# Kernel tuning notes

Measured on AMD Instinct MI355X. Metric: run time of the kernel, lower is better.

The kernel has to match this reference:

```python
import jax, jax.numpy as jnp
from jax import lax
import numpy as np

STRIDE = 16
PRE_NMS = 2000
POST_NMS = 300
NMS_THRESH = 0.7
MIN_SIZE = 16.0  # * img_scale (=1.0)
DN = ('NCHW', 'OIHW', 'NCHW')


def _anchor_base(base=16, ratios=(0.5, 1.0, 2.0), scales=(8, 16, 32)):
    py = px = base / 2.0
    ab = np.zeros((len(ratios) * len(scales), 4), np.float32)
    k = 0
    for r in ratios:
        for s in scales:
            h = base * s * np.sqrt(r)
            w = base * s * np.sqrt(1.0 / r)
            ab[k] = [py - h / 2, px - w / 2, py + h / 2, px + w / 2]
            k += 1
    return ab


def _all_anchors(H, W, img_h, img_w):
    base = _anchor_base()
    sy = np.arange(H, dtype=np.float32) * STRIDE
    sx = np.arange(W, dtype=np.float32) * STRIDE
    yy, xx = np.meshgrid(sy, sx, indexing='ij')
    shifts = np.stack([yy, xx, yy, xx], axis=-1).reshape(-1, 1, 4)
    anchors = (shifts + base[None]).reshape(-1, 4).astype(np.float32)  # (H*W*9, 4)
    valid = np.where((anchors[:, 0] >= 0) & (anchors[:, 1] >= 0) &
                     (anchors[:, 2] <= img_h) & (anchors[:, 3] <= img_w))[0]
    return anchors, valid


def _loc2bbox(anc, loc):
    # anc: (1,K,4), loc: (B,K,4); boxes as (y1,x1,y2,x2)
    h = anc[..., 2] - anc[..., 0]
    w = anc[..., 3] - anc[..., 1]
    cy = anc[..., 0] + 0.5 * h
    cx = anc[..., 1] + 0.5 * w
    ncy = loc[..., 0] * h + cy
    ncx = loc[..., 1] * w + cx
    nh = h * jnp.exp(loc[..., 2])
    nw = w * jnp.exp(loc[..., 3])
    return jnp.stack([ncy - 0.5 * nh, ncx - 0.5 * nw,
                      ncy + 0.5 * nh, ncx + 0.5 * nw], axis=-1)


def _nms(boxes, scores):
    # boxes: (N,4), scores: (N,) -> (POST_NMS,4) zero-padded rois
    areas = (boxes[:, 2] - boxes[:, 0]) * (boxes[:, 3] - boxes[:, 1])

    def step(s, _):
        i = jnp.argmax(s)
        ok = s[i] > -jnp.inf
        b = boxes[i]
        yy1 = jnp.maximum(b[0], boxes[:, 0])
        xx1 = jnp.maximum(b[1], boxes[:, 1])
        yy2 = jnp.minimum(b[2], boxes[:, 2])
        xx2 = jnp.minimum(b[3], boxes[:, 3])
        inter = jnp.maximum(yy2 - yy1, 0.0) * jnp.maximum(xx2 - xx1, 0.0)
        iou = inter / (areas[i] + areas - inter + 1e-9)
        s = jnp.where(iou > NMS_THRESH, -jnp.inf, s).at[i].set(-jnp.inf)
        return s, (i, ok)

    _, (idx, ok) = lax.scan(step, scores, None, length=POST_NMS)
    return boxes[idx] * ok[:, None].astype(boxes.dtype)


def _conv(x, w, b, padding):
    y = lax.conv_general_dilated(x, w, (1, 1), padding, dimension_numbers=DN)
    return y + b[None, :, None, None]


def setup_inputs():
    key = jax.random.key(0)
    k = jax.random.split(key, 4)
    B, C, H, W = 2, 512, 64, 64
    std = 0.01
    return {
        'feat': jax.random.normal(k[0], (B, C, H, W), jnp.float32),
        'share_w': jax.random.normal(k[1], (512, 512, 3, 3), jnp.float32) * std,
        'share_b': jnp.zeros((512,), jnp.float32),
        'cls_w': jax.random.normal(k[2], (18, 512, 1, 1), jnp.float32) * std,
        'cls_b': jnp.zeros((18,), jnp.float32),
        'reg_w': jax.random.normal(k[3], (36, 512, 1, 1), jnp.float32) * std,
        'reg_b': jnp.zeros((36,), jnp.float32),
        'img_h': 1024,
        'img_w': 1024,
    }


def reference(feat, share_w, share_b, cls_w, cls_b, reg_w, reg_b, img_h, img_w):
    B, _, H, W = feat.shape
    anchors_np, valid_np = _all_anchors(H, W, img_h, img_w)
    anchors = jnp.asarray(anchors_np)
    valid = jnp.asarray(valid_np)

    shared = jax.nn.relu(_conv(feat, share_w, share_b, 'SAME'))
    cls = _conv(shared, cls_w, cls_b, 'VALID')   # (B,18,H,W)
    reg = _conv(shared, reg_w, reg_b, 'VALID')   # (B,36,H,W)

    # permute(0,2,3,1).view(-1,2), gather valid anchors, softmax
    cls = cls.transpose(0, 2, 3, 1).reshape(B, -1, 2)[:, valid]   # (B,K,2)
    cls = jax.nn.softmax(cls, axis=-1)
    reg = reg.transpose(0, 2, 3, 1).reshape(B, -1, 4)[:, valid]   # (B,K,4)

    # proposal layer: decode, clip, min-size filter, top-k, NMS
    anc = anchors[valid][None]                                    # (1,K,4)
    boxes = _loc2bbox(anc, reg)                                   # (B,K,4)
    boxes = jnp.stack([jnp.clip(boxes[..., 0], 0.0, img_h),
                       jnp.clip(boxes[..., 1], 0.0, img_w),
                       jnp.clip(boxes[..., 2], 0.0, img_h),
                       jnp.clip(boxes[..., 3], 0.0, img_w)], axis=-1)
    hs = boxes[..., 2] - boxes[..., 0]
    ws = boxes[..., 3] - boxes[..., 1]
    scores = jnp.where((hs >= MIN_SIZE) & (ws >= MIN_SIZE), cls[..., 1], -jnp.inf)

    top_s, top_i = lax.top_k(scores, PRE_NMS)                     # (B,PRE_NMS)
    top_boxes = jnp.take_along_axis(boxes, top_i[..., None], axis=1)
    rois = jax.vmap(_nms)(top_boxes, top_s)                       # (B,POST_NMS,4)
    roi_list = rois.reshape(-1, 4)
    roi_id = jnp.repeat(jnp.arange(B, dtype=jnp.int32), POST_NMS)
    return cls, reg, roi_list, roi_id, anchors
```

## Files before the change

kernel.cpp:

```cpp
#include <hip/hip_runtime.h>
#include <math.h>

typedef unsigned int u32;
typedef unsigned long long u64;
typedef unsigned short ushort_t;

typedef __attribute__((ext_vector_type(8))) short short8;
typedef __attribute__((ext_vector_type(16))) float f32x16;

#define KANC 18376
#define PRE 2000
#define PREP 2048
#define POST 300

#define OUT_CLS 0
#define OUT_REG 73504
#define OUT_ROI 220512
#define OUT_RID 222912
#define OUT_ANC 223512

#define WS_NHWC   0u
#define WS_FT     16777216u
#define WS_W3     41943040u
#define WS_VPOS   56098816u
#define WS_BOXES  56246272u
#define WS_KEYS   56834304u
#define WS_TOPBOX 56981312u
#define WS_TOPKEY 57046848u
#define WS_MASK   57063232u

#define A_SPL2 7920

__device__ __forceinline__ ushort_t f2bf(float f) {
    u32 u = __float_as_uint(f);
    u32 r = (u + 0x7FFFu + ((u >> 16) & 1u)) >> 16;
    return (ushort_t)r;
}
__device__ __forceinline__ float bf2f(ushort_t h) {
    return __uint_as_float(((u32)h) << 16);
}
__device__ __forceinline__ u32 pack3(float v0, float v1, ushort_t* m0, ushort_t* m1,
                                     ushort_t* l0, ushort_t* l1) {
    ushort_t h0 = f2bf(v0);
    float r = v0 - bf2f(h0);
    *m0 = f2bf(r);
    *l0 = f2bf(r - bf2f(*m0));
    ushort_t h1 = f2bf(v1);
    float r1 = v1 - bf2f(h1);
    *m1 = f2bf(r1);
    *l1 = f2bf(r1 - bf2f(*m1));
    return (u32)h0 | ((u32)h1 << 16);
}

__device__ __forceinline__ void anchor_base(int t, float& y1, float& x1, float& y2, float& x2) {
    const double SQ[3] = {0.7071067811865476, 1.0, 1.4142135623730951};
    const double SC[3] = {8.0, 16.0, 32.0};
    int ri = t / 3, si = t % 3;
    double h = 16.0 * SC[si] * SQ[ri];
    double w = 16.0 * SC[si] * SQ[2 - ri];
    y1 = (float)(8.0 - h * 0.5);
    x1 = (float)(8.0 - w * 0.5);
    y2 = (float)(8.0 + h * 0.5);
    x2 = (float)(8.0 + w * 0.5);
}

__global__ __launch_bounds__(256) void t12_pre(const float* __restrict__ feat,
                                               const float* __restrict__ w,
                                               ushort_t* __restrict__ ft,
                                               ushort_t* __restrict__ w3,
                                               float* __restrict__ nhwc) {
    __shared__ float lds[8 * 577];
    int tid = threadIdx.x;
    int bid = blockIdx.x;
    if (bid < 1024) {
        float4 z4 = make_float4(0.f, 0.f, 0.f, 0.f);
        float4* nz = (float4*)nhwc + (size_t)bid * 1024;
        for (int i = tid; i < 1024; i += 256) nz[i] = z4;

        int by = bid >> 3;
        int b = by >> 6, y = by & 63;
        int ci0 = (bid & 7) * 64;
        for (int it = 0; it < 16; it++) {
            int idx = it * 256 + tid;
            int ci = idx >> 6, x = idx & 63;
            lds[ci * 65 + x] = feat[((size_t)(b * 512 + ci0 + ci) * 64 + y) * 64 + x];
        }
        __syncthreads();
        const size_t spl = (size_t)2 * 64 * 64 * 512;
        u32* ft32 = (u32*)ft;
        for (int it = 0; it < 8; it++) {
            int idx = it * 256 + tid;
            int x = idx >> 5, cp = idx & 31;
            float v0 = lds[(2 * cp) * 65 + x];
            float v1 = lds[(2 * cp + 1) * 65 + x];
            ushort_t m0, m1, l0, l1;
            u32 hi = pack3(v0, v1, &m0, &m1, &l0, &l1);
            size_t base = ((size_t)(b * 64 + y) * 64 + x) * 512 + ci0 + 2 * cp;
            ft32[base >> 1] = hi;
            ft32[(base + spl) >> 1] = (u32)m0 | ((u32)m1 << 16);
            ft32[(base + 2 * spl) >> 1] = (u32)l0 | ((u32)l1 << 16);
        }
    } else {
        int b2 = bid - 1024;
        int cob = b2 >> 3;
        int cib = (b2 & 7) * 64;
        for (int s = tid; s < 4608; s += 256) {
            int co = s / 576, r = s - co * 576;
            lds[co * 577 + r] = w[((size_t)(cob * 8 + co) * 512 + cib) * 9 + r];
        }
        __syncthreads();
        const size_t spl = (size_t)9 * 512 * 512;
        u32* w32 = (u32*)w3;
        int co = tid >> 5, cp = tid & 31;
        for (int kk = 0; kk < 9; kk++) {
            float v0 = lds[co * 577 + (2 * cp) * 9 + kk];
            float v1 = lds[co * 577 + (2 * cp + 1) * 9 + kk];
            ushort_t m0, m1, l0, l1;
            u32 hi = pack3(v0, v1, &m0, &m1, &l0, &l1);
            size_t base = ((size_t)kk * 512 + cob * 8 + co) * 512 + cib + 2 * cp;
            w32[base >> 1] = hi;
            w32[(base + spl) >> 1] = (u32)m0 | ((u32)m1 << 16);
            w32[(base + 2 * spl) >> 1] = (u32)l0 | ((u32)l1 << 16);
        }
    }
}

__global__ __launch_bounds__(256, 3) void k1_conv(const ushort_t* __restrict__ ft,
                                                  const ushort_t* __restrict__ w3,
                                                  float* __restrict__ nhwc) {
    __shared__ ushort_t lds16[3 * A_SPL2];
    int tid = threadIdx.x;
    int bid = blockIdx.x;
    int nt = bid & 1;
    int kh = (bid >> 1) & 3;
    int mt = bid >> 3;
    int b = mt >> 6, y = mt & 63;
    int nb = nt << 8;
    int ct0 = kh << 2;

    int lane = tid & 63;
    int w = tid >> 6;
    int wn = w << 6;
    int nlane = lane & 31;
    int kgrp8 = (lane >> 5) * 8;

    const size_t FT_SPL = (size_t)2 * 64 * 64 * 512;
    const size_t W3_SPL = (size_t)9 * 512 * 512;

    int sx = tid >> 2;
    int sq = tid & 3;

    f32x16 acc[2][2];
#pragma unroll
    for (int mi = 0; mi < 2; mi++)
#pragma unroll
        for (int ni = 0; ni < 2; ni++)
#pragma unroll
            for (int r = 0; r < 16; r++) acc[mi][ni][r] = 0.0f;

    if (tid < 72) {
        int s = tid / 24, rem = tid % 24;
        int r = rem >> 3, rem2 = rem & 7;
        int side = rem2 >> 2, q = rem2 & 3;
        uint4 z = make_uint4(0, 0, 0, 0);
        *(uint4*)&lds16[s * A_SPL2 + (r * 66 + side * 65) * 40 + q * 8] = z;
    }

    uint4 pbA[9];
    auto loadA = [&](int ct) {
#pragma unroll
        for (int r = 0; r < 3; r++) {
            int yy = y - 1 + r;
            bool valid = (yy >= 0 && yy < 64);
            size_t rowbase = ((size_t)(b * 64 + (valid ? yy : 0)) * 64 + sx) * 512 + ct * 32 + sq * 8;
#pragma unroll
            for (int s = 0; s < 3; s++) {
                uint4 v = make_uint4(0, 0, 0, 0);
                if (valid) v = *(const uint4*)&ft[rowbase + (size_t)s * FT_SPL];
                pbA[r * 3 + s] = v;
            }
        }
    };
    auto writeA = [&]() {
#pragma unroll
        for (int r = 0; r < 3; r++)
#pragma unroll
            for (int s = 0; s < 3; s++)
                *(uint4*)&lds16[s * A_SPL2 + (r * 66 + sx + 1) * 40 + sq * 8] = pbA[r * 3 + s];
    };

    short8 breg[2][2][3];
    auto loadB = [&](int buf, int tap, int ks, int ct) {
#pragma unroll
        for (int ni = 0; ni < 2; ni++) {
            size_t cobase = ((size_t)(tap * 512 + nb + wn + ni * 32 + nlane)) * 512
                            + ct * 32 + ks * 16 + kgrp8;
#pragma unroll
            for (int s = 0; s < 3; s++)
                breg[buf][ni][s] = *(const short8*)&w3[(size_t)s * W3_SPL + cobase];
        }
    };

    loadA(ct0);
    loadB(0, 0, 0, ct0);

    for (int ct = ct0; ct < ct0 + 4; ct++) {
        __syncthreads();
        writeA();
        __syncthreads();
        if (ct + 1 < ct0 + 4) loadA(ct + 1);

#pragma unroll
        for (int u = 0; u < 18; u++) {
            int cur = u & 1, alt = cur ^ 1;
            if (u + 1 < 18) loadB(alt, (u + 1) >> 1, (u + 1) & 1, ct);
            else if (ct + 1 < ct0 + 4) loadB(alt, 0, 0, ct + 1);
            int tap = u >> 1, ks = u & 1;
            int ky = tap / 3, kx = tap - ky * 3;

            short8 af[3][2];
#pragma unroll
            for (int s = 0; s < 3; s++) {
#pragma unroll
                for (int mi = 0; mi < 2; mi++)
                    af[s][mi] = *(const short8*)&lds16[s * A_SPL2 +
                        (ky * 66 + mi * 32 + nlane + kx) * 40 + ks * 16 + kgrp8];
            }
#pragma unroll
            for (int t = 0; t < 6; t++) {
                const int sa_t[6] = {0, 0, 1, 0, 1, 2};
                const int sb_t[6] = {0, 1, 0, 2, 1, 0};
                int sa = sa_t[t], sb = sb_t[t];
#pragma unroll
                for (int mi = 0; mi < 2; mi++)
#pragma unroll
                    for (int ni = 0; ni < 2; ni++)
                        acc[mi][ni] = __builtin_amdgcn_mfma_f32_32x32x16_bf16(
                            af[sa][mi], breg[cur][ni][sb], acc[mi][ni], 0, 0, 0);
            }
        }
    }

#pragma unroll
    for (int mi = 0; mi < 2; mi++) {
#pragma unroll
        for (int ni = 0; ni < 2; ni++) {
            int co = nb + wn + ni * 32 + nlane;
#pragma unroll
            for (int r = 0; r < 16; r++) {
                int xx = mi * 32 + (r & 3) + 8 * (r >> 2) + 4 * (lane >> 5);
                atomicAdd(&nhwc[((size_t)(b * 64 + y) * 64 + xx) * 512 + co], acc[mi][ni][r]);
            }
        }
    }
}

__global__ __launch_bounds__(256) void k2_heads(const float* __restrict__ nhwc,
                                                const float* __restrict__ share_b,
                                                const float* __restrict__ cls_w,
                                                const float* __restrict__ cls_b,
                                                const float* __restrict__ reg_w,
                                                const float* __restrict__ reg_b,
                                                float* __restrict__ out,
                                                float* __restrict__ boxes_ws,
                                                u32* __restrict__ keys_ws,
                                                const int* d_imgh, const int* d_imgw) {
    int bid = blockIdx.x;
    int row = bid >> 1;
    int b = row >> 6, y = row & 63;
    int h = bid & 1;
    int p0 = h * 32;
    int tid = threadIdx.x;
    __shared__ float Al[32 * 68];
    __shared__ float Wl[64 * 64];
    __shared__ float Ob[54 * 32];
    int og = tid & 15, pg = tid >> 4;
    float acc[2][4];
#pragma unroll
    for (int pp = 0; pp < 2; pp++)
#pragma unroll
        for (int j = 0; j < 4; j++) acc[pp][j] = 0.0f;

    for (int cib = 0; cib < 512; cib += 64) {
        for (int s = tid; s < 2048; s += 256) {
            int kk = s & 63, pp = s >> 6;
            float v = nhwc[((size_t)(b * 64 + y) * 64 + p0 + pp) * 512 + cib + kk]
                      + share_b[cib + kk];
            Al[pp * 68 + kk] = fmaxf(v, 0.0f);
        }
        for (int s = tid; s < 64 * 64; s += 256) {
            int o = s >> 6, kk = s & 63;
            float wv = 0.0f;
            if (o < 18) wv = cls_w[o * 512 + cib + kk];
            else if (o < 54) wv = reg_w[(o - 18) * 512 + cib + kk];
            Wl[s] = wv;
        }
        __syncthreads();
        for (int kq = 0; kq < 16; kq++) {
            float4 a0 = *(const float4*)&Al[(pg * 2) * 68 + kq * 4];
            float4 a1 = *(const float4*)&Al[(pg * 2 + 1) * 68 + kq * 4];
#pragma unroll
            for (int j = 0; j < 4; j++) {
                float4 w4 = *(const float4*)&Wl[(og * 4 + j) * 64 + kq * 4];
                acc[0][j] += a0.x * w4.x + a0.y * w4.y + a0.z * w4.z + a0.w * w4.w;
                acc[1][j] += a1.x * w4.x + a1.y * w4.y + a1.z * w4.z + a1.w * w4.w;
            }
        }
        __syncthreads();
    }
#pragma unroll
    for (int pp = 0; pp < 2; pp++)
#pragma unroll
        for (int j = 0; j < 4; j++) {
            int o = og * 4 + j;
            if (o < 54) {
                float bvv = (o < 18) ? cls_b[o] : reg_b[o - 18];
                Ob[o * 32 + pg * 2 + pp] = acc[pp][j] + bvv;
            }
        }
    __syncthreads();
    float imgh = (float)d_imgh[0], imgw = (float)d_imgw[0];
    for (int task = tid; task < 288; task += 256) {
        int ta = task >> 5, p2 = task & 31;
        int x = p0 + p2;
        int a_idx = (y * 64 + x) * 9 + ta;
        int j = 0;
        bool myvalid = false;
#pragma unroll
        for (int tt = 0; tt < 9; tt++) {
            float c0, c1, c2, c3;
            anchor_base(tt, c0, c1, c2, c3);
            int ylo = (int)((-c0) / 16.0f) + 1;
            int yhi = (int)((imgh - c2) / 16.0f);
            int xlo = (int)((-c1) / 16.0f) + 1;
            int xhi = (int)((imgw - c3) / 16.0f);
            ylo = max(ylo, 0); yhi = min(yhi, 63);
            xlo = max(xlo, 0); xhi = min(xhi, 63);
            int Wt  = max(xhi - xlo + 1, 0);
            int nry = max(yhi - ylo + 1, 0);
            int rb  = min(max(y - ylo, 0), nry);
            bool vy = (y >= ylo) && (y <= yhi);
            int cb  = vy ? min(max(x - xlo, 0), Wt) : 0;
            bool val = vy && (x >= xlo) && (x <= xhi);
            j += rb * Wt + cb + ((tt < ta && val) ? 1 : 0);
            if (tt == ta) {
                myvalid = val;
                float4 o4;
                o4.x = c0 + 16.0f * y;
                o4.y = c1 + 16.0f * x;
                o4.z = c2 + 16.0f * y;
                o4.w = c3 + 16.0f * x;
                *(float4*)&out[OUT_ANC + a_idx * 4] = o4;
            }
        }
        if (!myvalid) continue;
        float c0 = Ob[(2 * ta) * 32 + p2], c1 = Ob[(2 * ta + 1) * 32 + p2];
        float m = fmaxf(c0, c1);
        float e0 = expf(c0 - m), e1 = expf(c1 - m);
        float sden = e0 + e1;
        float p0v = e0 / sden, p1v = e1 / sden;
        out[OUT_CLS + (size_t)(b * KANC + j) * 2 + 0] = p0v;
        out[OUT_CLS + (size_t)(b * KANC + j) * 2 + 1] = p1v;
        float l0 = Ob[(18 + 4 * ta + 0) * 32 + p2];
        float l1 = Ob[(18 + 4 * ta + 1) * 32 + p2];
        float l2 = Ob[(18 + 4 * ta + 2) * 32 + p2];
        float l3 = Ob[(18 + 4 * ta + 3) * 32 + p2];
        out[OUT_REG + (size_t)(b * KANC + j) * 4 + 0] = l0;
        out[OUT_REG + (size_t)(b * KANC + j) * 4 + 1] = l1;
        out[OUT_REG + (size_t)(b * KANC + j) * 4 + 2] = l2;
        out[OUT_REG + (size_t)(b * KANC + j) * 4 + 3] = l3;
        float b0, b1, b2, b3; anchor_base(ta, b0, b1, b2, b3);
        float ay1 = b0 + 16.0f * y, ax1 = b1 + 16.0f * x;
        float ay2 = b2 + 16.0f * y, ax2 = b3 + 16.0f * x;
        float hh = ay2 - ay1, wdt = ax2 - ax1;
        float cy = ay1 + 0.5f * hh, cx = ax1 + 0.5f * wdt;
        float ncy = l0 * hh + cy, ncx = l1 * wdt + cx;
        float nh = hh * expf(l2), nw = wdt * expf(l3);
        float by1 = fminf(fmaxf(ncy - 0.5f * nh, 0.0f), imgh);
        float bx1 = fminf(fmaxf(ncx - 0.5f * nw, 0.0f), imgw);
        float by2 = fminf(fmaxf(ncy + 0.5f * nh, 0.0f), imgh);
        float bx2 = fminf(fmaxf(ncx + 0.5f * nw, 0.0f), imgw);
        boxes_ws[(size_t)(b * KANC + j) * 4 + 0] = by1;
        boxes_ws[(size_t)(b * KANC + j) * 4 + 1] = bx1;
        boxes_ws[(size_t)(b * KANC + j) * 4 + 2] = by2;
        boxes_ws[(size_t)(b * KANC + j) * 4 + 3] = bx2;
        float hs = by2 - by1, wsz = bx2 - bx1;
        u32 key = 0;
        if (hs >= 16.0f && wsz >= 16.0f) key = __float_as_uint(p1v) + 1u;
        keys_ws[b * KANC + j] = key;
    }
}

__device__ __forceinline__ void suffix_scan(u32* suf, const u32* hist, int N, int tid) {
    for (int i = tid; i < N; i += 1024) suf[i] = hist[i];
    if (tid == 0) suf[N] = 0;
    __syncthreads();
    for (int off = 1; off < N; off <<= 1) {
        u32 add0 = 0, add1 = 0;
        int i0 = tid, i1 = tid + 1024;
        if (i0 < N) add0 = (i0 + off < N) ? suf[i0 + off] : 0;
        if (i1 < N) add1 = (i1 + off < N) ? suf[i1 + off] : 0;
        __syncthreads();
        if (i0 < N) suf[i0] += add0;
        if (i1 < N) suf[i1] += add1;
        __syncthreads();
    }
}

__global__ __launch_bounds__(1024) void k3_select(const u32* __restrict__ keys_ws,
                                                  const float* __restrict__ boxes_ws,
                                                  u32* __restrict__ topkey,
                                                  float* __restrict__ topbox) {
    int b = blockIdx.x, tid = threadIdx.x;
    const u32* keys = keys_ws + (size_t)b * KANC;
    __shared__ u32 hist[2048];
    __shared__ u32 suf[2049];
    __shared__ int Ps;
    __shared__ int cnt;
    __shared__ u64 sbuf[2048];

    for (int i = tid; i < 2048; i += 1024) hist[i] = 0;
    __syncthreads();
    for (int i = tid; i < KANC; i += 1024) atomicAdd(&hist[keys[i] >> 20], 1u);
    __syncthreads();
    suffix_scan(suf, hist, 2048, tid);
    if (tid == 0) Ps = 0;
    __syncthreads();
    for (int i = tid; i < 2048; i += 1024)
        if (suf[i] >= (u32)PRE && suf[i + 1] < (u32)PRE) Ps = i;
    __syncthreads();
    u32 P1 = (u32)Ps;
    u32 quota2 = (u32)PRE - suf[P1 + 1];
    __syncthreads();

    for (int i = tid; i < 1024; i += 1024) hist[i] = 0;
    __syncthreads();
    for (int i = tid; i < KANC; i += 1024) {
        u32 k = keys[i];
        if ((k >> 20) == P1) atomicAdd(&hist[(k >> 10) & 1023u], 1u);
    }
    __syncthreads();
    suffix_scan(suf, hist, 1024, tid);
    if (tid == 0) Ps = 0;
    __syncthreads();
    for (int i = tid; i < 1024; i += 1024)
        if (suf[i] >= quota2 && suf[i + 1] < quota2) Ps = i;
    __syncthreads();
    u32 P2 = (u32)Ps;
    u32 quota3 = quota2 - suf[P2 + 1];
    __syncthreads();

    u32 pref = (P1 << 10) | P2;
    for (int i = tid; i < 1024; i += 1024) hist[i] = 0;
    __syncthreads();
    for (int i = tid; i < KANC; i += 1024) {
        u32 k = keys[i];
        if ((k >> 10) == pref) atomicAdd(&hist[k & 1023u], 1u);
    }
    __syncthreads();
    suffix_scan(suf, hist, 1024, tid);
    if (tid == 0) Ps = 0;
    __syncthreads();
    for (int i = tid; i < 1024; i += 1024)
        if (suf[i] >= quota3 && suf[i + 1] < quota3) Ps = i;
    __syncthreads();
    u32 P3 = (u32)Ps;
    u32 T = (P1 << 20) | (P2 << 10) | P3;
    u32 Tm = (T < 1u) ? 1u : T;

    for (int i = tid; i < 2048; i += 1024) sbuf[i] = 0ull;
    if (tid == 0) cnt = 0;
    __syncthreads();
    for (int i = tid; i < KANC; i += 1024) {
        u32 k = keys[i];
        if (k >= Tm) {
            int pos = atomicAdd(&cnt, 1);
            if (pos < 2048)
                sbuf[pos] = ((u64)k << 32) | (u64)(0xFFFFFFFFu - (u32)i);
        }
    }
    __syncthreads();

    for (int k2 = 2; k2 <= 2048; k2 <<= 1) {
        for (int j2 = k2 >> 1; j2 > 0; j2 >>= 1) {
            for (int i = tid; i < 2048; i += 1024) {
                int ixj = i ^ j2;
                if (ixj > i) {
                    u64 va = sbuf[i], vb = sbuf[ixj];
                    bool descRegion = ((i & k2) == 0);
                    if (descRegion ? (va < vb) : (va > vb)) {
                        sbuf[i] = vb; sbuf[ixj] = va;
                    }
                }
            }
            __syncthreads();
        }
    }

    for (int i = tid; i < PREP; i += 1024) {
        u64 v = sbuf[i];
        u32 kk = (u32)(v >> 32);
        u32 j = 0xFFFFFFFFu - (u32)(v & 0xFFFFFFFFull);
        bool good = (i < PRE) && (kk != 0);
        topkey[b * PREP + i] = good ? kk : 0;
        float4 bx = make_float4(0.0f, 0.0f, 0.0f, 0.0f);
        if (good) bx = *(const float4*)&boxes_ws[(size_t)(b * KANC + j) * 4];
        *(float4*)&topbox[(size_t)(b * PREP + i) * 4] = bx;
    }
}

__global__ __launch_bounds__(64) void k4_mask(const float* __restrict__ topbox,
                                              u64* __restrict__ mask) {
    int jb = blockIdx.x, ib = blockIdx.y, b = blockIdx.z;
    int lane = threadIdx.x;
    float4 bi = *(const float4*)&topbox[(size_t)(b * PREP + ib * 64 + lane) * 4];
    float4 bj = *(const float4*)&topbox[(size_t)(b * PREP + jb * 64 + lane) * 4];
    float ai = (bi.z - bi.x) * (bi.w - bi.y);
    float aj = (bj.z - bj.x) * (bj.w - bj.y);
    u64 word = 0;
    for (int ii = 0; ii < 64; ii++) {
        float y1 = __shfl(bi.x, ii), x1 = __shfl(bi.y, ii);
        float y2 = __shfl(bi.z, ii), x2 = __shfl(bi.w, ii);
        float aii = __shfl(ai, ii);
        float yy1 = fmaxf(y1, bj.x), xx1 = fmaxf(x1, bj.y);
        float yy2 = fminf(y2, bj.z), xx2 = fminf(x2, bj.w);
        float inter = fmaxf(yy2 - yy1, 0.0f) * fmaxf(xx2 - xx1, 0.0f);
        float iou = inter / (aii + aj - inter + 1e-9f);
        u64 bal = __ballot(iou > 0.7f);
        if (lane == ii) word = bal;
    }
    mask[(size_t)(b * PREP + ib * 64 + lane) * 32 + jb] = word;
}

__global__ __launch_bounds__(64) void k5_nms(const u32* __restrict__ topkey,
                                             const float* __restrict__ topbox,
                                             const u64* __restrict__ mask,
                                             float* __restrict__ out) {
    int b = blockIdx.x;
    int lane = threadIdx.x;
    __shared__ int kept[POST];

    u64 validw = 0;
    for (int it = 0; it < 32; it++) {
        u64 wv = __ballot(topkey[b * PREP + it * 64 + lane] != 0);
        if (lane == it) validw = wv;
    }

    const u64* mb = mask + (size_t)b * PREP * 32;
    u64 remv = 0;
    const int CH = 16;
    u64 bufA[CH], bufB[CH];
    auto loadRows = [&](u64* buf, int base) {
#pragma unroll
        for (int k = 0; k < CH; k++)
            buf[k] = (lane < 32) ? mb[(size_t)(base + k) * 32 + lane] : 0ull;
    };
    int nk = 0;
    auto process = [&](u64* buf, int base) {
        int wi = base >> 6, sh = base & 63;
        u64 supw = __shfl(remv, wi);
        u64 valw = __shfl(validw, wi);
        u32 cand = (u32)(((~supw & valw) >> sh) & 0xFFFFull);
        while (cand) {
            int k = __builtin_ctz(cand);
            cand &= cand - 1;
            int i = base + k;
            remv |= buf[k];
            u64 rw = __shfl(buf[k], wi);
            cand &= ~((u32)((rw >> sh) & 0xFFFFull));
            if (lane == 0) kept[nk] = i;
            nk++;
            if (nk == POST) break;
        }
    };

    loadRows(bufA, 0);
    for (int base = 0; base < PRE && nk < POST; base += 2 * CH) {
        loadRows(bufB, base + CH);
        process(bufA, base);
        if (nk < POST && base + CH < PRE) {
            if (base + 2 * CH < PRE) loadRows(bufA, base + 2 * CH);
            process(bufB, base + CH);
        }
    }
    __syncthreads();
    for (int s = lane; s < POST; s += 64) {
        float4 bx = make_float4(0.0f, 0.0f, 0.0f, 0.0f);
        if (s < nk) bx = *(const float4*)&topbox[(size_t)(b * PREP + kept[s]) * 4];
        *(float4*)&out[OUT_ROI + (size_t)(b * POST + s) * 4] = bx;
        out[OUT_RID + b * POST + s] = (float)b;
    }
}

extern "C" void kernel_launch(void* const* d_in, const int* in_sizes, int n_in,
                              void* d_out, int out_size, void* d_ws, size_t ws_size,
                              hipStream_t stream) {
    (void)in_sizes; (void)n_in; (void)out_size; (void)ws_size;
    const float* feat    = (const float*)d_in[0];
    const float* share_w = (const float*)d_in[1];
    const float* share_b = (const float*)d_in[2];
    const float* cls_w   = (const float*)d_in[3];
    const float* cls_b   = (const float*)d_in[4];
    const float* reg_w   = (const float*)d_in[5];
    const float* reg_b   = (const float*)d_in[6];
    const int*   imgh    = (const int*)d_in[7];
    const int*   imgw    = (const int*)d_in[8];
    float* out = (float*)d_out;
    char* ws = (char*)d_ws;
    float*     nhwc   = (float*)(ws + WS_NHWC);
    ushort_t*  ft     = (ushort_t*)(ws + WS_FT);
    ushort_t*  w3     = (ushort_t*)(ws + WS_W3);
    float*     boxes  = (float*)(ws + WS_BOXES);
    u32*       keys   = (u32*)(ws + WS_KEYS);
    float*     topbox = (float*)(ws + WS_TOPBOX);
    u32*       topkey = (u32*)(ws + WS_TOPKEY);
    u64*       maskp  = (u64*)(ws + WS_MASK);

    t12_pre<<<1536, 256, 0, stream>>>(feat, share_w, ft, w3, nhwc);
    k1_conv<<<1024, 256, 0, stream>>>(ft, w3, nhwc);
    k2_heads<<<256, 256, 0, stream>>>(nhwc, share_b, cls_w, cls_b, reg_w, reg_b,
                                      out, boxes, keys, imgh, imgw);
    k3_select<<<2, 1024, 0, stream>>>(keys, boxes, topkey, topbox);
    k4_mask<<<dim3(32, 32, 2), 64, 0, stream>>>(topbox, maskp);
    k5_nms<<<2, 64, 0, stream>>>(topkey, topbox, maskp, out);
}
```

Before: 673.0 us.

## Retile conv kernel to half-row x tiles with deeper K split per block

The 3x3 conv kernel now tiles the output row into two 32-pixel halves and splits the input channels into two groups of 8 chunks instead of four groups of 4, keeping the grid size the same. Each block holds a smaller LDS A tile and a single M fragment, so it uses fewer accumulator registers and less LDS, and the launch bound is raised to 4 blocks per CU for more occupancy. Halving the K split also halves the atomicAdd traffic into the fp32 output per element. The trade-off is that each block does half the MFMAs per B-fragment load, so weight reuse from registers drops and global weight traffic per MFMA roughly doubles, with extra halo loads per x tile.

```diff
diff --git a/kernel.cpp b/kernel.cpp
--- a/kernel.cpp
+++ b/kernel.cpp
@@ -29,7 +29,7 @@
 #define WS_TOPKEY 57046848u
 #define WS_MASK   57063232u
 
-#define A_SPL2 7920
+#define A_XSPL 4080
 
 __device__ __forceinline__ ushort_t f2bf(float f) {
     u32 u = __float_as_uint(f);
@@ -125,18 +125,20 @@
     }
 }
 
-__global__ __launch_bounds__(256, 3) void k1_conv(const ushort_t* __restrict__ ft,
+__global__ __launch_bounds__(256, 4) void k1_conv(const ushort_t* __restrict__ ft,
                                                   const ushort_t* __restrict__ w3,
                                                   float* __restrict__ nhwc) {
-    __shared__ ushort_t lds16[3 * A_SPL2];
+    __shared__ ushort_t lds16[3 * A_XSPL];
     int tid = threadIdx.x;
     int bid = blockIdx.x;
     int nt = bid & 1;
-    int kh = (bid >> 1) & 3;
+    int kh = (bid >> 1) & 1;
+    int xh = (bid >> 2) & 1;
     int mt = bid >> 3;
     int b = mt >> 6, y = mt & 63;
     int nb = nt << 8;
-    int ct0 = kh << 2;
+    int x0 = xh << 5;
+    int ct0 = kh << 3;
 
     int lane = tid & 63;
     int w = tid >> 6;
@@ -147,46 +149,41 @@
     const size_t FT_SPL = (size_t)2 * 64 * 64 * 512;
     const size_t W3_SPL = (size_t)9 * 512 * 512;
 
-    int sx = tid >> 2;
-    int sq = tid & 3;
-
-    f32x16 acc[2][2];
-#pragma unroll
-    for (int mi = 0; mi < 2; mi++)
-#pragma unroll
-        for (int ni = 0; ni < 2; ni++)
-#pragma unroll
-            for (int r = 0; r < 16; r++) acc[mi][ni][r] = 0.0f;
-
-    if (tid < 72) {
-        int s = tid / 24, rem = tid % 24;
-        int r = rem >> 3, rem2 = rem & 7;
-        int side = rem2 >> 2, q = rem2 & 3;
-        uint4 z = make_uint4(0, 0, 0, 0);
-        *(uint4*)&lds16[s * A_SPL2 + (r * 66 + side * 65) * 40 + q * 8] = z;
-    }
-
-    uint4 pbA[9];
+    f32x16 acc[2];
+#pragma unroll
+    for (int ni = 0; ni < 2; ni++)
+#pragma unroll
+        for (int r = 0; r < 16; r++) acc[ni][r] = 0.0f;
+
+    uint4 pbA[5];
     auto loadA = [&](int ct) {
 #pragma unroll
-        for (int r = 0; r < 3; r++) {
-            int yy = y - 1 + r;
-            bool valid = (yy >= 0 && yy < 64);
-            size_t rowbase = ((size_t)(b * 64 + (valid ? yy : 0)) * 64 + sx) * 512 + ct * 32 + sq * 8;
-#pragma unroll
-            for (int s = 0; s < 3; s++) {
-                uint4 v = make_uint4(0, 0, 0, 0);
-                if (valid) v = *(const uint4*)&ft[rowbase + (size_t)s * FT_SPL];
-                pbA[r * 3 + s] = v;
+        for (int k5 = 0; k5 < 5; k5++) {
+            int s = tid + k5 * 256;
+            uint4 v = make_uint4(0, 0, 0, 0);
+            if (s < 1224) {
+                int spl = s / 408, rem = s - spl * 408;
+                int r = rem / 136, rem2 = rem - r * 136;
+                int xi = rem2 >> 2, sq = rem2 & 3;
+                int yy = y - 1 + r, x = x0 - 1 + xi;
+                if (yy >= 0 && yy < 64 && x >= 0 && x < 64)
+                    v = *(const uint4*)&ft[(size_t)spl * FT_SPL +
+                        (((size_t)(b * 64 + yy) * 64 + x) * 512 + ct * 32 + sq * 8)];
             }
+            pbA[k5] = v;
         }
     };
     auto writeA = [&]() {
 #pragma unroll
-        for (int r = 0; r < 3; r++)
-#pragma unroll
-            for (int s = 0; s < 3; s++)
-                *(uint4*)&lds16[s * A_SPL2 + (r * 66 + sx + 1) * 40 + sq * 8] = pbA[r * 3 + s];
+        for (int k5 = 0; k5 < 5; k5++) {
+            int s = tid + k5 * 256;
+            if (s < 1224) {
+                int spl = s / 408, rem = s - spl * 408;
+                int r = rem / 136, rem2 = rem - r * 136;
+                int xi = rem2 >> 2, sq = rem2 & 3;
+                *(uint4*)&lds16[spl * A_XSPL + r * 1360 + xi * 40 + sq * 8] = pbA[k5];
+            }
+        }
     };
 
     short8 breg[2][2][3];
@@ -204,53 +201,45 @@
     loadA(ct0);
     loadB(0, 0, 0, ct0);
 
-    for (int ct = ct0; ct < ct0 + 4; ct++) {
+    for (int ct = ct0; ct < ct0 + 8; ct++) {
         __syncthreads();
         writeA();
         __syncthreads();
-        if (ct + 1 < ct0 + 4) loadA(ct + 1);
+        if (ct + 1 < ct0 + 8) loadA(ct + 1);
 
 #pragma unroll
         for (int u = 0; u < 18; u++) {
             int cur = u & 1, alt = cur ^ 1;
             if (u + 1 < 18) loadB(alt, (u + 1) >> 1, (u + 1) & 1, ct);
-            else if (ct + 1 < ct0 + 4) loadB(alt, 0, 0, ct + 1);
+            else if (ct + 1 < ct0 + 8) loadB(alt, 0, 0, ct + 1);
             int tap = u >> 1, ks = u & 1;
             int ky = tap / 3, kx = tap - ky * 3;
 
-            short8 af[3][2];
-#pragma unroll
-            for (int s = 0; s < 3; s++) {
-#pragma unroll
-                for (int mi = 0; mi < 2; mi++)
-                    af[s][mi] = *(const short8*)&lds16[s * A_SPL2 +
-                        (ky * 66 + mi * 32 + nlane + kx) * 40 + ks * 16 + kgrp8];
-            }
+            short8 af[3];
+#pragma unroll
+            for (int s = 0; s < 3; s++)
+                af[s] = *(const short8*)&lds16[s * A_XSPL +
+                    ky * 1360 + (nlane + kx) * 40 + ks * 16 + kgrp8];
 #pragma unroll
             for (int t = 0; t < 6; t++) {
                 const int sa_t[6] = {0, 0, 1, 0, 1, 2};
                 const int sb_t[6] = {0, 1, 0, 2, 1, 0};
                 int sa = sa_t[t], sb = sb_t[t];
 #pragma unroll
-                for (int mi = 0; mi < 2; mi++)
-#pragma unroll
-                    for (int ni = 0; ni < 2; ni++)
-                        acc[mi][ni] = __builtin_amdgcn_mfma_f32_32x32x16_bf16(
-                            af[sa][mi], breg[cur][ni][sb], acc[mi][ni], 0, 0, 0);
+                for (int ni = 0; ni < 2; ni++)
+                    acc[ni] = __builtin_amdgcn_mfma_f32_32x32x16_bf16(
+                        af[sa], breg[cur][ni][sb], acc[ni], 0, 0, 0);
             }
         }
     }
 
 #pragma unroll
-    for (int mi = 0; mi < 2; mi++) {
-#pragma unroll
-        for (int ni = 0; ni < 2; ni++) {
-            int co = nb + wn + ni * 32 + nlane;
-#pragma unroll
-            for (int r = 0; r < 16; r++) {
-                int xx = mi * 32 + (r & 3) + 8 * (r >> 2) + 4 * (lane >> 5);
-                atomicAdd(&nhwc[((size_t)(b * 64 + y) * 64 + xx) * 512 + co], acc[mi][ni][r]);
-            }
+    for (int ni = 0; ni < 2; ni++) {
+        int co = nb + wn + ni * 32 + nlane;
+#pragma unroll
+        for (int r = 0; r < 16; r++) {
+            int x = x0 + (r & 3) + 8 * (r >> 2) + 4 * (lane >> 5);
+            atomicAdd(&nhwc[((size_t)(b * 64 + y) * 64 + x) * 512 + co], acc[ni][r]);
         }
     }
 }
```

Result: slower. 881.8 us (+31.0%).
